# Optimization experiments

Measured on AMD Instinct MI355X. Metric: run time of the kernel, lower is better.

Reference implementation:

```python
import jax, jax.numpy as jnp
import numpy as np

HIDDEN = 4096
N_HEADS = 32
N_KV_HEADS = 8
HEAD_SIZE = HIDDEN // N_HEADS  # 128
ROPE_THETA = 10000.0
SEQ_LEN = 1024
BATCH = 4


def setup_inputs() -> dict:
    key = jax.random.key(0)
    k1, k2, k3 = jax.random.split(key, 3)
    scale = 1.0 / np.sqrt(HIDDEN)
    hidden_states = jax.random.normal(k1, (BATCH * SEQ_LEN, HIDDEN), dtype=jnp.float32)
    w_qkv = jax.random.normal(k2, ((N_HEADS + 2 * N_KV_HEADS) * HEAD_SIZE, HIDDEN), dtype=jnp.float32) * scale
    w_o = jax.random.normal(k3, (HIDDEN, N_HEADS * HEAD_SIZE), dtype=jnp.float32) * scale
    return {"hidden_states": hidden_states, "w_qkv": w_qkv, "w_o": w_o, "seq_len": SEQ_LEN}


def _rope(x, pos, theta):
    # x: [B, S, H, D]; pos: [S] absolute positions; rotate-half (LLAMA/NeoX) style
    d = x.shape[-1]
    inv_freq = 1.0 / (theta ** (jnp.arange(0, d, 2, dtype=jnp.float32) / d))  # [D/2]
    ang = pos.astype(jnp.float32)[:, None] * inv_freq[None, :]  # [S, D/2]
    cos = jnp.cos(ang)[None, :, None, :]
    sin = jnp.sin(ang)[None, :, None, :]
    x1, x2 = jnp.split(x, 2, axis=-1)
    return jnp.concatenate([x1 * cos - x2 * sin, x2 * cos + x1 * sin], axis=-1)


def reference(hidden_states, w_qkv, w_o, seq_len):
    total, hidden = hidden_states.shape
    B = total // seq_len
    hd = HEAD_SIZE
    # fused QKV projection (bias-free), split like the torch module
    qkv = hidden_states @ w_qkv.T  # [T, (H+2K)*hd]
    q, k, v = jnp.split(qkv, [N_HEADS * hd, (N_HEADS + N_KV_HEADS) * hd], axis=1)
    q = q.reshape(B, seq_len, N_HEADS, hd)
    k = k.reshape(B, seq_len, N_KV_HEADS, hd)
    v = v.reshape(B, seq_len, N_KV_HEADS, hd)
    # inline RoPE (ROPE_LLAMA) on q and k at absolute positions
    pos = jnp.arange(seq_len)
    q = _rope(q, pos, ROPE_THETA)
    k = _rope(k, pos, ROPE_THETA)
    # GQA: map each q head to its kv head (kv_head_mapping = repeat_interleave)
    groups = N_HEADS // N_KV_HEADS
    k = jnp.repeat(k, groups, axis=2)  # [B, S, H, hd]
    v = jnp.repeat(v, groups, axis=2)
    scale = hd ** -0.5
    scores = jnp.einsum('bqhd,bkhd->bhqk', q, k) * scale  # [B, H, S, S]
    causal = jnp.tril(jnp.ones((seq_len, seq_len), dtype=bool))
    scores = jnp.where(causal[None, None], scores, jnp.finfo(scores.dtype).min)
    probs = jax.nn.softmax(scores, axis=-1)
    attn = jnp.einsum('bhqk,bkhd->bqhd', probs, v).reshape(total, N_HEADS * hd)
    return attn @ w_o.T  # [T, hidden]
```

## Files before the change

kernel.cpp:

```cpp
#include <hip/hip_runtime.h>


typedef short bf16x8 __attribute__((ext_vector_type(8)));
typedef short bf16x4 __attribute__((ext_vector_type(4)));
typedef float floatx4 __attribute__((ext_vector_type(4)));
typedef unsigned short u16x4 __attribute__((ext_vector_type(4)));

__device__ __forceinline__ unsigned short f2bf(float f) {
  unsigned u = __float_as_uint(f);
  u += 0x7FFFu + ((u >> 16) & 1u);
  return (unsigned short)(u >> 16);
}
__device__ __forceinline__ float bf2f(unsigned short h) {
  return __uint_as_float(((unsigned)h) << 16);
}

__device__ __forceinline__ void async16(const void* g, void* l) {
  __builtin_amdgcn_global_load_lds(
      (const __attribute__((address_space(1))) unsigned int*)g,
      (__attribute__((address_space(3))) unsigned int*)l, 16, 0, 0);
}

__global__ void cvt_xw(const float4* __restrict__ X,
                       const float4* __restrict__ Wq,
                       u16x4* __restrict__ Xb, u16x4* __restrict__ Wqb) {
  const float4* src;
  u16x4* dst;
  int j;
  if (blockIdx.x < 16384) {
    src = X; dst = Xb; j = blockIdx.x * 256 + threadIdx.x;
  } else {
    src = Wq; dst = Wqb; j = (blockIdx.x - 16384) * 256 + threadIdx.x;
  }
  float4 v = src[j];
  u16x4 o;
  o.x = f2bf(v.x); o.y = f2bf(v.y); o.z = f2bf(v.z); o.w = f2bf(v.w);
  dst[j] = o;
}

__global__ void cvt_f32_bf16(const float4* __restrict__ in,
                             u16x4* __restrict__ out, int n4) {
  int i = blockIdx.x * 256 + threadIdx.x;
  if (i < n4) {
    float4 v = in[i];
    u16x4 o;
    o.x = f2bf(v.x); o.y = f2bf(v.y); o.z = f2bf(v.z); o.w = f2bf(v.w);
    out[i] = o;
  }
}

template <int OUT_BF16>
__global__ __launch_bounds__(512, 2) void gemm256(
    const unsigned short* __restrict__ A, const unsigned short* __restrict__ B,
    void* __restrict__ Cout, int M, int N, int K) {
  __shared__ __align__(16) unsigned short As[4][8192];
  __shared__ __align__(16) unsigned short Bs[4][8192];
  const int tid = threadIdx.x;
  const int wave = tid >> 6, lane = tid & 63;
  const int wm = wave >> 2, wn = wave & 3;
  const int l16 = lane & 15, c4 = lane >> 4;
  const int bm = blockIdx.y << 8, bn = blockIdx.x << 8;

  int afOff[8], bfOff[4];
#pragma unroll
  for (int mi = 0; mi < 8; ++mi) {
    int r = wm * 128 + mi * 16 + l16;
    int pr = r >> 1, l8 = ((r & 1) << 2) | c4;
    afOff[mi] = pr * 128 + ((l8 ^ (pr & 7)) << 4);
  }
#pragma unroll
  for (int ni = 0; ni < 4; ++ni) {
    int r = wn * 64 + ni * 16 + l16;
    int pr = r >> 1, l8 = ((r & 1) << 2) | c4;
    bfOff[ni] = pr * 128 + ((l8 ^ (pr & 7)) << 4);
  }

  const int sp = lane >> 3;
  const int l8s = (lane & 7) ^ sp;
  const int so = l8s >> 2, sc = (l8s & 3) << 3;
  const unsigned short* aS0 = A + (size_t)(bm + wave * 16 + sp * 2 + so) * K + sc;
  const unsigned short* aS1 = A + (size_t)(bm + (wave + 8) * 16 + sp * 2 + so) * K + sc;
  const unsigned short* bS0 = B + (size_t)(bn + wave * 16 + sp * 2 + so) * K + sc;
  const unsigned short* bS1 = B + (size_t)(bn + (wave + 8) * 16 + sp * 2 + so) * K + sc;
  const int dst0 = wave * 1024, dst1 = (wave + 8) * 1024;

  floatx4 acc[8][4];
#pragma unroll
  for (int mi = 0; mi < 8; ++mi)
#pragma unroll
    for (int ni = 0; ni < 4; ++ni) acc[mi][ni] = (floatx4){0.f, 0.f, 0.f, 0.f};

  const int NT = K >> 5;
  async16(aS0, (char*)As[0] + dst0);
  async16(aS1, (char*)As[0] + dst1);
  async16(bS0, (char*)Bs[0] + dst0);
  async16(bS1, (char*)Bs[0] + dst1);
  async16(aS0 + 32, (char*)As[1] + dst0);
  async16(aS1 + 32, (char*)As[1] + dst1);
  async16(bS0 + 32, (char*)Bs[1] + dst0);
  async16(bS1 + 32, (char*)Bs[1] + dst1);
  asm volatile("s_waitcnt vmcnt(4)" ::: "memory");
  __builtin_amdgcn_s_barrier();

  bf16x8 afq0[4], afq1[4], bfc[4];
#pragma unroll
  for (int i = 0; i < 4; ++i)
    afq0[i] = *(const bf16x8*)((const char*)As[0] + afOff[i]);
#pragma unroll
  for (int i = 0; i < 4; ++i)
    bfc[i] = *(const bf16x8*)((const char*)Bs[0] + bfOff[i]);

  size_t koff = 64;
  for (int t = 0; t < NT; ++t) {
    const char* aB = (const char*)As + ((size_t)(t & 3) << 14);
    const char* aN = (const char*)As + ((size_t)((t + 1) & 3) << 14);
    const char* bN = (const char*)Bs + ((size_t)((t + 1) & 3) << 14);
    char* aD = (char*)As + ((size_t)((t + 2) & 3) << 14);
    char* bD = (char*)Bs + ((size_t)((t + 2) & 3) << 14);

    __builtin_amdgcn_s_setprio(1);
#pragma unroll
    for (int mi = 0; mi < 4; ++mi)
#pragma unroll
      for (int ni = 0; ni < 4; ++ni)
        acc[mi][ni] = __builtin_amdgcn_mfma_f32_16x16x32_bf16(
            afq0[mi], bfc[ni], acc[mi][ni], 0, 0, 0);
    __builtin_amdgcn_s_setprio(0);
#pragma unroll
    for (int i = 0; i < 4; ++i)
      afq1[i] = *(const bf16x8*)(aB + afOff[4 + i]);
    async16(aS0 + koff, aD + dst0);
    async16(aS1 + koff, aD + dst1);
    async16(bS0 + koff, bD + dst0);
    async16(bS1 + koff, bD + dst1);
    asm volatile("s_waitcnt vmcnt(4)" ::: "memory");
    __builtin_amdgcn_s_barrier();

    __builtin_amdgcn_s_setprio(1);
#pragma unroll
    for (int mi = 0; mi < 4; ++mi)
#pragma unroll
      for (int ni = 0; ni < 4; ++ni)
        acc[4 + mi][ni] = __builtin_amdgcn_mfma_f32_16x16x32_bf16(
            afq1[mi], bfc[ni], acc[4 + mi][ni], 0, 0, 0);
    __builtin_amdgcn_s_setprio(0);
#pragma unroll
    for (int i = 0; i < 4; ++i)
      afq0[i] = *(const bf16x8*)(aN + afOff[i]);
#pragma unroll
    for (int i = 0; i < 4; ++i)
      bfc[i] = *(const bf16x8*)(bN + bfOff[i]);
    __builtin_amdgcn_s_barrier();
    koff += 32;
  }

  const int col0 = bn + wn * 64 + l16;
#pragma unroll
  for (int mi = 0; mi < 8; ++mi) {
    const int row0 = bm + wm * 128 + mi * 16 + c4 * 4;
#pragma unroll
    for (int ni = 0; ni < 4; ++ni)
#pragma unroll
      for (int r = 0; r < 4; ++r) {
        if (OUT_BF16)
          ((unsigned short*)Cout)[(size_t)(row0 + r) * N + col0 + ni * 16] =
              f2bf(acc[mi][ni][r]);
        else
          ((float*)Cout)[(size_t)(row0 + r) * N + col0 + ni * 16] =
              acc[mi][ni][r];
      }
  }
}

__global__ void rope_k_kernel(unsigned short* __restrict__ qkv) {
  const int t = blockIdx.x;
  const int s = t & 1023;
  const int head = 32 + blockIdx.y * 4 + (threadIdx.x >> 6);
  const int d = threadIdx.x & 63;
  unsigned short* p = qkv + (size_t)t * 6144 + head * 128;
  float x1 = bf2f(p[d]), x2 = bf2f(p[d + 64]);
  float inv_freq = exp2f((float)d * -0.20762050593046015f);
  float ang = (float)s * inv_freq;
  float c, sn;
  __sincosf(ang, &sn, &c);
  p[d] = f2bf(x1 * c - x2 * sn);
  p[d + 64] = f2bf(x2 * c + x1 * sn);
}

__global__ __launch_bounds__(256, 3) void flash_attn(
    const unsigned short* __restrict__ qkv, unsigned short* __restrict__ aout) {
  const int pr = blockIdx.x;
  const int h = blockIdx.y, b = blockIdx.z;
  const int kh = h >> 2;
  const int tid = threadIdx.x;
  const int wave = tid >> 6, lane = tid & 63;
  const int quad = lane >> 4, l16 = lane & 15;

  __shared__ __align__(16) unsigned short Ks[64][136];
  __shared__ __align__(16) unsigned short Vt[128][68];
  __shared__ __align__(16) unsigned short Ps[64][68];

  const int krow = tid >> 4, kcol = (tid & 15) << 3;
  const int vrb = (tid & 15) << 2, vcol = (tid >> 4) << 3;
  const unsigned short* kp = qkv + (size_t)(b << 10) * 6144 + 4096 + kh * 128;
  const unsigned short* vp = qkv + (size_t)(b << 10) * 6144 + 5120 + kh * 128;

  for (int half = 0; half < 2; ++half) {
    const int qt = half ? pr : 15 - pr;
    const int q0 = qt << 6;

    bf16x8 qf[4];
    {
      const int qrow = q0 + wave * 16 + l16;
      const unsigned short* qp =
          qkv + (size_t)((b << 10) + qrow) * 6144 + h * 128 + quad * 8;
#pragma unroll
      for (int ks = 0; ks < 4; ++ks) qf[ks] = *(const bf16x8*)(qp + ks * 32);
      const float pos = (float)qrow;
      const float scale = 0.08838834764831845f;
#pragma unroll
      for (int ks = 0; ks < 2; ++ks)
#pragma unroll
        for (int e = 0; e < 8; ++e) {
          int d = ks * 32 + quad * 8 + e;
          float ang = pos * exp2f((float)d * -0.20762050593046015f);
          float c, sn;
          __sincosf(ang, &sn, &c);
          float x1 = bf2f((unsigned short)qf[ks][e]);
          float x2 = bf2f((unsigned short)qf[ks + 2][e]);
          qf[ks][e] = (short)f2bf((x1 * c - x2 * sn) * scale);
          qf[ks + 2][e] = (short)f2bf((x2 * c + x1 * sn) * scale);
        }
    }

    floatx4 o_acc[8];
#pragma unroll
    for (int i = 0; i < 8; ++i) o_acc[i] = (floatx4){0.f, 0.f, 0.f, 0.f};
    float l_lane[4] = {0.f, 0.f, 0.f, 0.f};

    bf16x8 kreg[4], vreg[4];
#pragma unroll
    for (int j = 0; j < 4; ++j)
      kreg[j] = *(const bf16x8*)(kp + (size_t)(krow + j * 16) * 6144 + kcol);
#pragma unroll
    for (int j = 0; j < 4; ++j)
      vreg[j] = *(const bf16x8*)(vp + (size_t)(vrb + j) * 6144 + vcol);

    for (int t = 0; t <= qt; ++t) {
      __syncthreads();
#pragma unroll
      for (int j = 0; j < 4; ++j)
        *(bf16x8*)&Ks[krow + j * 16][kcol] = kreg[j];
#pragma unroll
      for (int e = 0; e < 8; ++e) {
        bf16x4 w = {vreg[0][e], vreg[1][e], vreg[2][e], vreg[3][e]};
        *(bf16x4*)&Vt[vcol + e][vrb] = w;
      }
      __syncthreads();
      if (t < qt) {
        const size_t nb = (size_t)((t + 1) << 6) * 6144;
#pragma unroll
        for (int j = 0; j < 4; ++j)
          kreg[j] =
              *(const bf16x8*)(kp + nb + (size_t)(krow + j * 16) * 6144 + kcol);
#pragma unroll
        for (int j = 0; j < 4; ++j)
          vreg[j] = *(const bf16x8*)(vp + nb + (size_t)(vrb + j) * 6144 + vcol);
      }

      floatx4 sacc[4];
#pragma unroll
      for (int ni = 0; ni < 4; ++ni) sacc[ni] = (floatx4){0.f, 0.f, 0.f, 0.f};
#pragma unroll
      for (int ks = 0; ks < 4; ++ks)
#pragma unroll
        for (int ni = 0; ni < 4; ++ni) {
          bf16x8 kf = *(const bf16x8*)&Ks[ni * 16 + l16][ks * 32 + quad * 8];
          sacc[ni] = __builtin_amdgcn_mfma_f32_16x16x32_bf16(qf[ks], kf,
                                                             sacc[ni], 0, 0, 0);
        }

      const bool masked = (t == qt);
#pragma unroll
      for (int r = 0; r < 4; ++r) {
        float rs = 0.f;
#pragma unroll
        for (int ni = 0; ni < 4; ++ni) {
          float e = __expf(sacc[ni][r]);
          if (masked && (ni * 16 + l16) > (wave * 16 + quad * 4 + r)) e = 0.f;
          rs += e;
          Ps[wave * 16 + quad * 4 + r][ni * 16 + l16] = f2bf(e);
        }
        l_lane[r] += rs;
      }
      asm volatile("s_waitcnt lgkmcnt(0)" ::: "memory");

#pragma unroll
      for (int ks2 = 0; ks2 < 2; ++ks2) {
        bf16x8 pf = *(const bf16x8*)&Ps[wave * 16 + l16][ks2 * 32 + quad * 8];
#pragma unroll
        for (int n8 = 0; n8 < 8; ++n8) {
          bf16x8 vf = *(const bf16x8*)&Vt[n8 * 16 + l16][ks2 * 32 + quad * 8];
          o_acc[n8] = __builtin_amdgcn_mfma_f32_16x16x32_bf16(pf, vf, o_acc[n8],
                                                              0, 0, 0);
        }
      }
    }

#pragma unroll
    for (int r = 0; r < 4; ++r) {
      float l = l_lane[r];
#pragma unroll
      for (int off = 1; off < 16; off <<= 1) l += __shfl_xor(l, off, 64);
      float inv = 1.0f / l;
      int row = q0 + wave * 16 + quad * 4 + r;
      unsigned short* op = aout + (size_t)((b << 10) + row) * 4096 + h * 128;
#pragma unroll
      for (int n8 = 0; n8 < 8; ++n8)
        op[n8 * 16 + l16] = f2bf(o_acc[n8][r] * inv);
    }
  }
}

extern "C" void kernel_launch(void* const* d_in, const int* in_sizes, int n_in,
                              void* d_out, int out_size, void* d_ws,
                              size_t ws_size, hipStream_t stream) {
  const float* X = (const float*)d_in[0];
  const float* Wqkv = (const float*)d_in[1];
  const float* Wo = (const float*)d_in[2];
  (void)in_sizes; (void)n_in; (void)out_size; (void)ws_size;

  char* ws = (char*)d_ws;
  unsigned short* Wqkvb = (unsigned short*)ws;
  unsigned short* AttnB = (unsigned short*)ws;
  unsigned short* Xb = (unsigned short*)(ws + 50331648);
  unsigned short* Wob = (unsigned short*)(ws + 50331648);
  unsigned short* QKVb = (unsigned short*)(ws + 83886080);

  cvt_xw<<<40960, 256, 0, stream>>>((const float4*)X, (const float4*)Wqkv,
                                    (u16x4*)Xb, (u16x4*)Wqkvb);
  gemm256<1><<<dim3(24, 16), 512, 0, stream>>>(Xb, Wqkvb, QKVb, 4096, 6144, 4096);
  rope_k_kernel<<<dim3(4096, 2), 256, 0, stream>>>(QKVb);
  cvt_f32_bf16<<<16384, 256, 0, stream>>>((const float4*)Wo, (u16x4*)Wob, 4194304);
  flash_attn<<<dim3(8, 32, 4), 256, 0, stream>>>(QKVb, AttnB);
  gemm256<0><<<dim3(16, 16), 512, 0, stream>>>(AttnB, Wob, d_out, 4096, 4096, 4096);
}
```

Measured before the change: 687.3 us.

## Restructure GEMM main loop into barrier-separated phases with split async loads

Rewrites the bf16 GEMM K-loop as four phases per two k-tiles, each loading fragments from LDS, issuing half of the next tile's global-to-LDS copies, waiting on lgkmcnt, then running 16 MFMAs at raised priority between workgroup barriers. This drops the register double-buffering of A fragments (afq0/afq1) in favour of reloading each phase, and spreads async loads across phases. The aim is to interleave memory and MFMA work across the waves, but it adds barriers and full LDS waits before every MFMA block, which may expose LDS latency. The loop assumes NT is even.

```diff
diff --git a/kernel.cpp b/kernel.cpp
--- a/kernel.cpp
+++ b/kernel.cpp
@@ -48,6 +48,27 @@
     out[i] = o;
   }
 }
+
+#define MFQ(Q)                                                               \
+  _Pragma("unroll") for (int mi = 0; mi < 4; ++mi)                           \
+      _Pragma("unroll") for (int ni = 0; ni < 4; ++ni)                       \
+          acc[(Q) * 4 + mi][ni] = __builtin_amdgcn_mfma_f32_16x16x32_bf16(   \
+              af[mi], bfc[ni], acc[(Q) * 4 + mi][ni], 0, 0, 0);
+
+#define PHASE_HEAD()                                                         \
+  __builtin_amdgcn_s_barrier();                                              \
+  asm volatile("s_waitcnt lgkmcnt(0)" ::: "memory");                         \
+  __builtin_amdgcn_sched_barrier(0);                                         \
+  __builtin_amdgcn_s_setprio(1);
+
+#define PHASE_TAIL()                                                         \
+  __builtin_amdgcn_s_setprio(0);                                             \
+  __builtin_amdgcn_s_barrier();
+
+#define PHASE_TAIL_VM()                                                      \
+  __builtin_amdgcn_s_setprio(0);                                             \
+  asm volatile("s_waitcnt vmcnt(4)" ::: "memory");                           \
+  __builtin_amdgcn_s_barrier();
 
 template <int OUT_BF16>
 __global__ __launch_bounds__(512, 2) void gemm256(
@@ -102,56 +123,55 @@
   asm volatile("s_waitcnt vmcnt(4)" ::: "memory");
   __builtin_amdgcn_s_barrier();
 
-  bf16x8 afq0[4], afq1[4], bfc[4];
-#pragma unroll
-  for (int i = 0; i < 4; ++i)
-    afq0[i] = *(const bf16x8*)((const char*)As[0] + afOff[i]);
-#pragma unroll
-  for (int i = 0; i < 4; ++i)
-    bfc[i] = *(const bf16x8*)((const char*)Bs[0] + bfOff[i]);
-
+  bf16x8 af[4], bfc[4];
   size_t koff = 64;
-  for (int t = 0; t < NT; ++t) {
-    const char* aB = (const char*)As + ((size_t)(t & 3) << 14);
-    const char* aN = (const char*)As + ((size_t)((t + 1) & 3) << 14);
-    const char* bN = (const char*)Bs + ((size_t)((t + 1) & 3) << 14);
-    char* aD = (char*)As + ((size_t)((t + 2) & 3) << 14);
-    char* bD = (char*)Bs + ((size_t)((t + 2) & 3) << 14);
-
-    __builtin_amdgcn_s_setprio(1);
-#pragma unroll
-    for (int mi = 0; mi < 4; ++mi)
-#pragma unroll
-      for (int ni = 0; ni < 4; ++ni)
-        acc[mi][ni] = __builtin_amdgcn_mfma_f32_16x16x32_bf16(
-            afq0[mi], bfc[ni], acc[mi][ni], 0, 0, 0);
-    __builtin_amdgcn_s_setprio(0);
-#pragma unroll
-    for (int i = 0; i < 4; ++i)
-      afq1[i] = *(const bf16x8*)(aB + afOff[4 + i]);
-    async16(aS0 + koff, aD + dst0);
-    async16(aS1 + koff, aD + dst1);
-    async16(bS0 + koff, bD + dst0);
-    async16(bS1 + koff, bD + dst1);
-    asm volatile("s_waitcnt vmcnt(4)" ::: "memory");
-    __builtin_amdgcn_s_barrier();
-
-    __builtin_amdgcn_s_setprio(1);
-#pragma unroll
-    for (int mi = 0; mi < 4; ++mi)
-#pragma unroll
-      for (int ni = 0; ni < 4; ++ni)
-        acc[4 + mi][ni] = __builtin_amdgcn_mfma_f32_16x16x32_bf16(
-            afq1[mi], bfc[ni], acc[4 + mi][ni], 0, 0, 0);
-    __builtin_amdgcn_s_setprio(0);
-#pragma unroll
-    for (int i = 0; i < 4; ++i)
-      afq0[i] = *(const bf16x8*)(aN + afOff[i]);
-#pragma unroll
-    for (int i = 0; i < 4; ++i)
-      bfc[i] = *(const bf16x8*)(bN + bfOff[i]);
-    __builtin_amdgcn_s_barrier();
-    koff += 32;
+  for (int t = 0; t < NT; t += 2) {
+    const char* a0 = (const char*)As + ((size_t)(t & 3) << 14);
+    const char* b0 = (const char*)Bs + ((size_t)(t & 3) << 14);
+    const char* a1 = (const char*)As + ((size_t)((t + 1) & 3) << 14);
+    const char* b1 = (const char*)Bs + ((size_t)((t + 1) & 3) << 14);
+    char* aD0 = (char*)As + ((size_t)((t + 2) & 3) << 14);
+    char* bD0 = (char*)Bs + ((size_t)((t + 2) & 3) << 14);
+    char* aD1 = (char*)As + ((size_t)((t + 3) & 3) << 14);
+    char* bD1 = (char*)Bs + ((size_t)((t + 3) & 3) << 14);
+
+#pragma unroll
+    for (int i = 0; i < 4; ++i) af[i] = *(const bf16x8*)(a0 + afOff[i]);
+#pragma unroll
+    for (int i = 0; i < 4; ++i) bfc[i] = *(const bf16x8*)(b0 + bfOff[i]);
+    async16(aS0 + koff, aD0 + dst0);
+    async16(aS1 + koff, aD0 + dst1);
+    PHASE_HEAD();
+    MFQ(0);
+    PHASE_TAIL();
+
+#pragma unroll
+    for (int i = 0; i < 4; ++i) af[i] = *(const bf16x8*)(a0 + afOff[4 + i]);
+    async16(bS0 + koff, bD0 + dst0);
+    async16(bS1 + koff, bD0 + dst1);
+    PHASE_HEAD();
+    MFQ(1);
+    PHASE_TAIL_VM();
+
+#pragma unroll
+    for (int i = 0; i < 4; ++i) af[i] = *(const bf16x8*)(a1 + afOff[i]);
+#pragma unroll
+    for (int i = 0; i < 4; ++i) bfc[i] = *(const bf16x8*)(b1 + bfOff[i]);
+    async16(aS0 + koff + 32, aD1 + dst0);
+    async16(aS1 + koff + 32, aD1 + dst1);
+    PHASE_HEAD();
+    MFQ(0);
+    PHASE_TAIL();
+
+#pragma unroll
+    for (int i = 0; i < 4; ++i) af[i] = *(const bf16x8*)(a1 + afOff[4 + i]);
+    async16(bS0 + koff + 32, bD1 + dst0);
+    async16(bS1 + koff + 32, bD1 + dst1);
+    PHASE_HEAD();
+    MFQ(1);
+    PHASE_TAIL_VM();
+
+    koff += 64;
   }
 
   const int col0 = bn + wn * 64 + l16;
```

Measured after the change: 727.8 us. +5.9%, slower.
